# Optimization experiments

Measured on AMD Instinct MI355X. Metric: run time of the kernel, lower is better.

Reference implementation:

```python
import jax, jax.numpy as jnp
import numpy as np

DIM = 256      # dim
DSTATE = 16    # d_state
DCONV = 4      # d_conv
DINNER = 256   # expand=1 -> d_inner = dim (required for B/C Linear shapes to check)
BATCH = 4
NPTS = 4096


def setup_inputs() -> dict:
    key = jax.random.key(0)
    ks = jax.random.split(key, 12)
    s = 0.02
    return {
        "x":      jax.random.normal(ks[0], (BATCH, DIM, NPTS), jnp.float32),
        # in_proj: Conv1d(dim, 2*d_inner, 1)
        "w_in":   jax.random.normal(ks[1], (2 * DINNER, DIM), jnp.float32) * s,
        "b_in":   jnp.zeros((2 * DINNER,), jnp.float32),
        # depthwise conv: Conv1d(d_inner, d_inner, d_conv, groups=d_inner)
        "w_conv": jax.random.normal(ks[2], (DINNER, 1, DCONV), jnp.float32) * s,
        "b_conv": jnp.zeros((DINNER,), jnp.float32),
        # A param; sampled so |A| = exp(A_log) < 1 for a stable 4096-step recurrence
        "A_log":  -jax.random.uniform(ks[3], (DINNER, DSTATE), jnp.float32, 0.1, 3.0),
        "D_skip": jax.random.normal(ks[4], (DINNER,), jnp.float32),
        # B/C Linear(dim, d_state, bias=False) weights [d_state, dim]
        "Bw":     jax.random.normal(ks[5], (DSTATE, DIM), jnp.float32) * s,
        "Cw":     jax.random.normal(ks[6], (DSTATE, DIM), jnp.float32) * s,
        # out_proj: Conv1d(d_inner, dim, 1)
        "w_out":  jax.random.normal(ks[7], (DIM, DINNER), jnp.float32) * s,
        "b_out":  jnp.zeros((DIM,), jnp.float32),
        "gamma":  jnp.ones((DIM,), jnp.float32),
        "beta":   jnp.zeros((DIM,), jnp.float32),
    }


def _forward(x, w_in, b_in, w_conv, b_conv, A_log, D_skip, Bw, Cw, w_out, b_out, gamma, beta):
    B, C, N = x.shape
    residual = jnp.swapaxes(x, 1, 2)                       # [B,N,C]
    # 1x1 conv in_proj on [B,C,N]
    xp = jnp.einsum('bcn,oc->bon', x, w_in) + b_in[:, None]  # [B,2*Di,N]
    x1, z = jnp.split(xp, 2, axis=1)                       # each [B,Di,N]
    # depthwise causal conv (torch pad=d_conv-1 both sides then truncate [:N])
    xc = jax.lax.conv_general_dilated(
        x1, w_conv, window_strides=(1,), padding=[(DCONV - 1, 0)],
        feature_group_count=DINNER,
        dimension_numbers=('NCH', 'OIH', 'NCH')) + b_conv[:, None]
    xs = jax.nn.silu(xc)                                   # [B,Di,N]
    A = -jnp.exp(A_log)                                    # [Di,S]
    xT = jnp.swapaxes(xs, 1, 2)                            # [B,N,Di]
    Bm = xT @ Bw.T                                         # [B,N,S]
    Cm = xT @ Cw.T                                         # [B,N,S]
    delta = jax.nn.sigmoid(jnp.swapaxes(z, 1, 2))          # [B,N,Di]
    dB = delta[..., None] * Bm[:, :, None, :]              # [B,N,Di,S]

    def step(h, t):
        dB_t, C_t, x_t = t                                 # [B,Di,S],[B,S],[B,Di]
        h = A * h + dB_t                                   # diagonal SSM update
        y = jnp.einsum('bds,bs->bd', h, C_t) + D_skip * x_t
        return h, y

    h0 = jnp.zeros((B, DINNER, DSTATE), x.dtype)
    _, ys = jax.lax.scan(
        step, h0,
        (jnp.swapaxes(dB, 0, 1), jnp.swapaxes(Cm, 0, 1), jnp.swapaxes(xT, 0, 1)))
    x_ssm = jnp.transpose(ys, (1, 2, 0))                   # [B,Di,N]
    out = jnp.einsum('bdn,cd->bcn', x_ssm, w_out) + b_out[:, None]  # [B,C,N]
    out = jnp.swapaxes(out, 1, 2) + residual               # [B,N,C]
    mu = out.mean(-1, keepdims=True)
    var = out.var(-1, keepdims=True)
    out = (out - mu) / jnp.sqrt(var + 1e-5) * gamma + beta  # LayerNorm over C
    return jnp.swapaxes(out, 1, 2)                          # [B,C,N]


def reference(x, w_in, b_in, w_conv, b_conv, A_log, D_skip, Bw, Cw, w_out, b_out, gamma, beta):
    return _forward(x, w_in, b_in, w_conv, b_conv, A_log, D_skip, Bw, Cw, w_out, b_out, gamma, beta)
```

## Files before the change

kernel.cpp:

```cpp
#include <hip/hip_runtime.h>
#include <math.h>

#define NPTS 4096
#define LDA  264
#define S_R1  0
#define S_DT  18480
#define S_BML 35376
#define S_CML 37936
#define SMEM_SZ 40496

typedef __bf16 bf16x8 __attribute__((ext_vector_type(8)));
typedef __bf16 bf16x4 __attribute__((ext_vector_type(4)));
typedef float  f32x4  __attribute__((ext_vector_type(4)));
typedef float  f32x2  __attribute__((ext_vector_type(2)));

#define PK_MUL(d, s0, s1)  asm("v_pk_mul_f32 %0, %1, %2" : "=v"(d) : "v"(s0), "v"(s1))
#define PK_FMA(d, s0, s2)  asm("v_pk_fma_f32 %0, %1, %0, %2" : "+v"(d) : "v"(s0), "v"(s2))
#define PK_FMA3(d, s0, s1) asm("v_pk_fma_f32 %0, %1, %2, %0" : "+v"(d) : "v"(s0), "v"(s1))

__device__ __forceinline__ float sigmoidf_(float v) {
  return __fdividef(1.f, 1.f + __expf(-v));
}
__device__ __forceinline__ f32x2 lo2(float4 v) { f32x2 r; r[0] = v.x; r[1] = v.y; return r; }
__device__ __forceinline__ f32x2 hi2(float4 v) { f32x2 r; r[0] = v.z; r[1] = v.w; return r; }

__global__ __launch_bounds__(256) void k_prep(const float* __restrict__ w_in,
                                              const float* __restrict__ w_out,
                                              const float* __restrict__ Bw,
                                              const float* __restrict__ Cw,
                                              __bf16* __restrict__ wbi,
                                              __bf16* __restrict__ wbo,
                                              __bf16* __restrict__ wbB,
                                              __bf16* __restrict__ wbC) {
  int i = blockIdx.x * 256 + threadIdx.x;
  const float* src; __bf16* dst; int off;
  if (i < 32768)      { src = w_in;  dst = wbi; off = i; }
  else if (i < 49152) { src = w_out; dst = wbo; off = i - 32768; }
  else if (i < 50176) { src = Bw;    dst = wbB; off = i - 49152; }
  else                { src = Cw;    dst = wbC; off = i - 50176; }
  float4 v = *(const float4*)&src[off << 2];
  bf16x4 p;
  p[0] = (__bf16)v.x; p[1] = (__bf16)v.y; p[2] = (__bf16)v.z; p[3] = (__bf16)v.w;
  *(bf16x4*)&dst[off << 2] = p;
}

__global__ __launch_bounds__(512, 4) void k_partA(const float* __restrict__ x,
                                                  const __bf16* __restrict__ wbi,
                                                  const float* __restrict__ b_in,
                                                  const float* __restrict__ wconv,
                                                  const float* __restrict__ bconv,
                                                  const float* __restrict__ A_log,
                                                  const __bf16* __restrict__ wbB,
                                                  const __bf16* __restrict__ wbC,
                                                  __bf16* __restrict__ dG,
                                                  __bf16* __restrict__ xsG,
                                                  float* __restrict__ BGg,
                                                  float* __restrict__ CGg,
                                                  float* __restrict__ E) {
  extern __shared__ unsigned char smem[];
  __bf16* R1  = (__bf16*)(smem + S_R1);
  __bf16* bdt = (__bf16*)(smem + S_DT);
  float*  Bml = (float*) (smem + S_BML);
  float*  Cml = (float*) (smem + S_CML);

  const int tid = threadIdx.x, lane = tid & 63, w = tid >> 6;
  const int b = blockIdx.y, cx = blockIdx.x, t0 = cx << 5;
  const int mrow = lane & 15, klane = (lane >> 4) << 3;
  const int r4 = (lane >> 4) << 2;
  const int ds = tid >> 1, sh = (tid & 1) << 3;

  f32x2 a01, a23, a45, a67;
  {
    float4 A0 = *(const float4*)&A_log[(ds << 4) + sh];
    float4 A1 = *(const float4*)&A_log[(ds << 4) + sh + 4];
    a01[0] = -__expf(A0.x); a01[1] = -__expf(A0.y);
    a23[0] = -__expf(A0.z); a23[1] = -__expf(A0.w);
    a45[0] = -__expf(A1.x); a45[1] = -__expf(A1.y);
    a67[0] = -__expf(A1.z); a67[1] = -__expf(A1.w);
  }

  {
    const int c = tid >> 1;
    const size_t xrow = (size_t)(b * 256 + c) * NPTS;
    #pragma unroll
    for (int r = 0; r < 4; ++r) {
      int fg = (tid & 1) + (r << 1);
      int t = t0 + (fg << 2);
      float4 v = *(const float4*)&x[xrow + t];
      int i0 = 3 + (fg << 2);
      R1[(i0 + 0) * LDA + c] = (__bf16)v.x;
      R1[(i0 + 1) * LDA + c] = (__bf16)v.y;
      R1[(i0 + 2) * LDA + c] = (__bf16)v.z;
      R1[(i0 + 3) * LDA + c] = (__bf16)v.w;
    }
    if (tid < 256) {
      int t = t0 - 4;
      float4 v = make_float4(0.f, 0.f, 0.f, 0.f);
      if (t >= 0) v = *(const float4*)&x[(size_t)(b * 256 + tid) * NPTS + t];
      R1[0 * LDA + tid] = (__bf16)v.y;
      R1[1 * LDA + tid] = (__bf16)v.z;
      R1[2 * LDA + tid] = (__bf16)v.w;
    }
  }
  const __bf16* wZ0 = &wbi[(size_t)(256 + (w << 5) + mrow) * 256 + klane];
  const __bf16* wZ1 = wZ0 + 16 * 256;
  bf16x8 z0v = *(const bf16x8*)&wZ0[0];
  bf16x8 z1v = *(const bf16x8*)&wZ1[0];
  __syncthreads();

  {
    f32x4 acc[2][2] = {};
    for (int k0 = 0; k0 < 256; k0 += 32) {
      bf16x8 af0 = z0v, af1 = z1v;
      int kn = (k0 + 32) & 255;
      z0v = *(const bf16x8*)&wZ0[kn];
      z1v = *(const bf16x8*)&wZ1[kn];
      #pragma unroll
      for (int ni = 0; ni < 2; ++ni) {
        bf16x8 bx = *(bf16x8*)&R1[(3 + (ni << 4) + mrow) * LDA + k0 + klane];
        acc[0][ni] = __builtin_amdgcn_mfma_f32_16x16x32_bf16(af0, bx, acc[0][ni], 0, 0, 0);
        acc[1][ni] = __builtin_amdgcn_mfma_f32_16x16x32_bf16(af1, bx, acc[1][ni], 0, 0, 0);
      }
    }
    #pragma unroll
    for (int mi = 0; mi < 2; ++mi) {
      int d = (w << 5) + (mi << 4) + r4;
      float4 bi = *(const float4*)&b_in[256 + d];
      float bia[4] = {bi.x, bi.y, bi.z, bi.w};
      #pragma unroll
      for (int ni = 0; ni < 2; ++ni) {
        int j = (ni << 4) + mrow;
        bf16x4 p;
        #pragma unroll
        for (int rg = 0; rg < 4; ++rg)
          p[rg] = (__bf16)sigmoidf_(acc[mi][ni][rg] + bia[rg]);
        *(bf16x4*)&bdt[j * LDA + d] = p;
      }
    }
  }

  {
    const __bf16* wX0 = &wbi[(size_t)((w << 5) + mrow) * 256 + klane];
    const __bf16* wX1 = wX0 + 16 * 256;
    bf16x8 x0v = *(const bf16x8*)&wX0[0];
    bf16x8 x1v = *(const bf16x8*)&wX1[0];
    f32x4 acc[2][3] = {};
    const int n0s[3] = {0, 16, 19};
    for (int k0 = 0; k0 < 256; k0 += 32) {
      bf16x8 af0 = x0v, af1 = x1v;
      int kn = (k0 + 32) & 255;
      x0v = *(const bf16x8*)&wX0[kn];
      x1v = *(const bf16x8*)&wX1[kn];
      #pragma unroll
      for (int ni = 0; ni < 3; ++ni) {
        bf16x8 bx = *(bf16x8*)&R1[(n0s[ni] + mrow) * LDA + k0 + klane];
        acc[0][ni] = __builtin_amdgcn_mfma_f32_16x16x32_bf16(af0, bx, acc[0][ni], 0, 0, 0);
        acc[1][ni] = __builtin_amdgcn_mfma_f32_16x16x32_bf16(af1, bx, acc[1][ni], 0, 0, 0);
      }
    }
    __syncthreads();
    #pragma unroll
    for (int mi = 0; mi < 2; ++mi) {
      int d = (w << 5) + (mi << 4) + r4;
      float4 bi = *(const float4*)&b_in[d];
      float bia[4] = {bi.x, bi.y, bi.z, bi.w};
      #pragma unroll
      for (int ni = 0; ni < 3; ++ni) {
        int i = n0s[ni] + mrow;
        bool ok = (t0 - 3 + i) >= 0;
        bf16x4 p;
        #pragma unroll
        for (int rg = 0; rg < 4; ++rg) {
          float v = acc[mi][ni][rg] + bia[rg];
          p[rg] = ok ? (__bf16)v : (__bf16)0.f;
        }
        *(bf16x4*)&R1[i * LDA + d] = p;
      }
    }
  }
  #pragma unroll
  for (int r = 0; r < 2; ++r) {
    int idx = (r << 9) + tid;
    int row = idx >> 5, colg = (idx & 31) << 3;
    *(uint4*)&dG[((size_t)(b * NPTS + t0 + row)) * 256 + colg] =
        *(uint4*)&bdt[row * LDA + colg];
  }
  __syncthreads();

  const int mat = w >> 1, n0bc = (w & 1) << 4;
  const __bf16* WrBC = (mat ? wbC : wbB) + mrow * 256 + klane;
  bf16x8 wv = {};
  if (w < 4) wv = *(const bf16x8*)&WrBC[0];

  {
    const int d = tid & 255, seg = tid >> 8;
    const int j0 = seg << 4;
    const float4 wc = *(const float4*)&wconv[d << 2];
    const float bcv = bconv[d];
    float m3 = (float)R1[(j0 + 0) * LDA + d];
    float m2 = (float)R1[(j0 + 1) * LDA + d];
    float m1 = (float)R1[(j0 + 2) * LDA + d];
    float xc_n = (float)R1[(j0 + 3) * LDA + d];
    float d0 = 0.f, d1 = 0.f, d2 = 0.f;
    #pragma unroll
    for (int i2 = 0; i2 < 16; ++i2) {
      float xc = xc_n;
      xc_n = (float)R1[(j0 + (i2 == 15 ? 18 : i2 + 4)) * LDA + d];
      float cv = fmaf(wc.x, m3, fmaf(wc.y, m2, fmaf(wc.z, m1, fmaf(wc.w, xc, bcv))));
      float sv = cv * sigmoidf_(cv);
      if (seg && i2 == 0)      d0 = sv;
      else if (seg && i2 == 1) d1 = sv;
      else if (seg && i2 == 2) d2 = sv;
      else R1[(j0 + i2) * LDA + d] = (__bf16)sv;
      m3 = m2; m2 = m1; m1 = xc;
    }
    __syncthreads();
    if (seg) {
      R1[(j0 + 0) * LDA + d] = (__bf16)d0;
      R1[(j0 + 1) * LDA + d] = (__bf16)d1;
      R1[(j0 + 2) * LDA + d] = (__bf16)d2;
    }
  }
  __syncthreads();

  if (w < 4) {
    f32x4 accb = {};
    for (int k0 = 0; k0 < 256; k0 += 32) {
      bf16x8 av = wv;
      int kn = (k0 + 32) & 255;
      wv = *(const bf16x8*)&WrBC[kn];
      bf16x8 bv = *(bf16x8*)&R1[(n0bc + mrow) * LDA + k0 + klane];
      accb = __builtin_amdgcn_mfma_f32_16x16x32_bf16(av, bv, accb, 0, 0, 0);
    }
    float* dst = mat ? Cml : Bml;
    int j = n0bc + mrow;
    #pragma unroll
    for (int rg = 0; rg < 4; ++rg)
      dst[j * 20 + r4 + rg] = accb[rg];
  } else {
    const int tid2 = tid - 256;
    #pragma unroll
    for (int r = 0; r < 4; ++r) {
      int idx = (r << 8) + tid2;
      int row = idx >> 5, colg = (idx & 31) << 3;
      *(uint4*)&xsG[((size_t)(b * NPTS + t0 + row)) * 256 + colg] =
          *(uint4*)&R1[row * LDA + colg];
    }
  }
  __syncthreads();

  {
    int j = tid >> 4, s = tid & 15;
    size_t gi = ((size_t)(b * 128 + cx) << 9) + tid;
    BGg[gi] = Bml[j * 20 + s];
    CGg[gi] = Cml[j * 20 + s];
  }

  f32x2 h01 = {0.f, 0.f}, h23 = {0.f, 0.f}, h45 = {0.f, 0.f}, h67 = {0.f, 0.f};
  {
    float u_n = (float)bdt[0 * LDA + ds];
    float4 b0_n = *(float4*)&Bml[0 * 20 + sh];
    float4 b1_n = *(float4*)&Bml[0 * 20 + sh + 4];
    #pragma unroll
    for (int j = 0; j < 32; ++j) {
      float u = u_n; float4 b0 = b0_n, b1 = b1_n;
      int jn = (j + 1) & 31;
      u_n = (float)bdt[jn * LDA + ds];
      b0_n = *(float4*)&Bml[jn * 20 + sh];
      b1_n = *(float4*)&Bml[jn * 20 + sh + 4];
      f32x2 u2; u2[0] = u; u2[1] = u;
      f32x2 t;
      PK_MUL(t, u2, lo2(b0)); PK_FMA(h01, a01, t);
      PK_MUL(t, u2, hi2(b0)); PK_FMA(h23, a23, t);
      PK_MUL(t, u2, lo2(b1)); PK_FMA(h45, a45, t);
      PK_MUL(t, u2, hi2(b1)); PK_FMA(h67, a67, t);
    }
  }
  {
    float* Ep = E + ((size_t)(b * 128 + cx) << 12) + (ds << 4) + sh;
    float4 e0, e1;
    e0.x = h01[0]; e0.y = h01[1]; e0.z = h23[0]; e0.w = h23[1];
    e1.x = h45[0]; e1.y = h45[1]; e1.z = h67[0]; e1.w = h67[1];
    *(float4*)&Ep[0] = e0;
    *(float4*)&Ep[4] = e1;
  }
}

__global__ __launch_bounds__(512, 4) void k_partB(const float* __restrict__ x,
                                                  const float* __restrict__ A_log,
                                                  const float* __restrict__ Dsk,
                                                  const __bf16* __restrict__ wbo,
                                                  const float* __restrict__ b_out,
                                                  const float* __restrict__ gamma,
                                                  const float* __restrict__ beta,
                                                  const __bf16* __restrict__ dG,
                                                  const __bf16* __restrict__ xsG,
                                                  const float* __restrict__ BGg,
                                                  const float* __restrict__ CGg,
                                                  const float* __restrict__ E,
                                                  float* __restrict__ out) {
  extern __shared__ unsigned char smem[];
  __bf16* R1  = (__bf16*)(smem + S_R1);
  __bf16* bdt = (__bf16*)(smem + S_DT);
  float*  Bml = (float*) (smem + S_BML);
  float*  Cml = (float*) (smem + S_CML);
  float*  Ct  = (float*) (smem + S_R1);

  const int tid = threadIdx.x, lane = tid & 63, w = tid >> 6;
  const int b = blockIdx.y, cx = blockIdx.x, t0 = cx << 5;
  const int mrow = lane & 15, klane = (lane >> 4) << 3;
  const int r4 = (lane >> 4) << 2;
  const int ds = tid >> 1, sh = (tid & 1) << 3;

  const __bf16* wO0 = &wbo[(size_t)((w << 5) + mrow) * 256 + klane];
  const __bf16* wO1 = wO0 + 16 * 256;
  bf16x8 o0v = *(const bf16x8*)&wO0[0];
  bf16x8 o1v = *(const bf16x8*)&wO1[0];

  #pragma unroll
  for (int r = 0; r < 2; ++r) {
    int idx = (r << 9) + tid;
    int row = idx >> 5, colg = (idx & 31) << 3;
    size_t gsrc = ((size_t)(b * NPTS + t0 + row)) * 256 + colg;
    *(uint4*)&bdt[row * LDA + colg] = *(const uint4*)&dG[gsrc];
    *(uint4*)&R1[row * LDA + colg]  = *(const uint4*)&xsG[gsrc];
  }
  {
    int j = tid >> 4, s = tid & 15;
    size_t gi = ((size_t)(b * 128 + cx) << 9) + tid;
    Bml[j * 20 + s] = BGg[gi];
    Cml[j * 20 + s] = CGg[gi];
  }

  f32x2 a01, a23, a45, a67, a32_01, a32_23, a32_45, a32_67;
  {
    float4 A0 = *(const float4*)&A_log[(ds << 4) + sh];
    float4 A1 = *(const float4*)&A_log[(ds << 4) + sh + 4];
    a01[0] = -__expf(A0.x); a01[1] = -__expf(A0.y);
    a23[0] = -__expf(A0.z); a23[1] = -__expf(A0.w);
    a45[0] = -__expf(A1.x); a45[1] = -__expf(A1.y);
    a67[0] = -__expf(A1.z); a67[1] = -__expf(A1.w);
    a32_01[0] = __expf(32.f * A0.x); a32_01[1] = __expf(32.f * A0.y);
    a32_23[0] = __expf(32.f * A0.z); a32_23[1] = __expf(32.f * A0.w);
    a32_45[0] = __expf(32.f * A1.x); a32_45[1] = __expf(32.f * A1.y);
    a32_67[0] = __expf(32.f * A1.z); a32_67[1] = __expf(32.f * A1.w);
  }
  const float Dv = Dsk[ds];

  f32x2 h01, h23, h45, h67;
  {
    const float* Eb = E + ((size_t)(b * 128) << 12) + (ds << 4) + sh;
    float4 z4 = make_float4(0.f, 0.f, 0.f, 0.f);
    float4 e1a = z4, e1b = z4, e2a = z4, e2b = z4, e3a = z4, e3b = z4;
    if (cx >= 1) { e1a = *(const float4*)&Eb[(size_t)(cx - 1) << 12];
                   e1b = *(const float4*)&Eb[((size_t)(cx - 1) << 12) + 4]; }
    if (cx >= 2) { e2a = *(const float4*)&Eb[(size_t)(cx - 2) << 12];
                   e2b = *(const float4*)&Eb[((size_t)(cx - 2) << 12) + 4]; }
    if (cx >= 3) { e3a = *(const float4*)&Eb[(size_t)(cx - 3) << 12];
                   e3b = *(const float4*)&Eb[((size_t)(cx - 3) << 12) + 4]; }
    f32x2 t01 = lo2(e2a); PK_FMA3(t01, a32_01, lo2(e3a));
    f32x2 t23 = hi2(e2a); PK_FMA3(t23, a32_23, hi2(e3a));
    f32x2 t45 = lo2(e2b); PK_FMA3(t45, a32_45, lo2(e3b));
    f32x2 t67 = hi2(e2b); PK_FMA3(t67, a32_67, hi2(e3b));
    h01 = lo2(e1a); PK_FMA3(h01, a32_01, t01);
    h23 = hi2(e1a); PK_FMA3(h23, a32_23, t23);
    h45 = lo2(e1b); PK_FMA3(h45, a32_45, t45);
    h67 = hi2(e1b); PK_FMA3(h67, a32_67, t67);
  }
  __syncthreads();

  {
    float u_n = (float)bdt[0 * LDA + ds];
    float4 b0_n = *(float4*)&Bml[0 * 20 + sh];
    float4 b1_n = *(float4*)&Bml[0 * 20 + sh + 4];
    float4 c0_n = *(float4*)&Cml[0 * 20 + sh];
    float4 c1_n = *(float4*)&Cml[0 * 20 + sh + 4];
    #pragma unroll
    for (int j = 0; j < 32; ++j) {
      float u = u_n; float4 b0 = b0_n, b1 = b1_n, c0 = c0_n, c1 = c1_n;
      int jn = (j + 1) & 31;
      u_n = (float)bdt[jn * LDA + ds];
      b0_n = *(float4*)&Bml[jn * 20 + sh];
      b1_n = *(float4*)&Bml[jn * 20 + sh + 4];
      c0_n = *(float4*)&Cml[jn * 20 + sh];
      c1_n = *(float4*)&Cml[jn * 20 + sh + 4];
      f32x2 u2; u2[0] = u; u2[1] = u;
      f32x2 t, pa, pb;
      PK_MUL(t, u2, lo2(b0)); PK_FMA(h01, a01, t);
      PK_MUL(t, u2, hi2(b0)); PK_FMA(h23, a23, t);
      PK_MUL(t, u2, lo2(b1)); PK_FMA(h45, a45, t);
      PK_MUL(t, u2, hi2(b1)); PK_FMA(h67, a67, t);
      PK_MUL(pa, h01, lo2(c0)); PK_FMA3(pa, h23, hi2(c0));
      PK_MUL(pb, h45, lo2(c1)); PK_FMA3(pb, h67, hi2(c1));
      float yv = pa[0] + pa[1] + pb[0] + pb[1];
      yv += __shfl_xor(yv, 1);
      if ((tid & 1) == 0) {
        float xv = (float)R1[j * LDA + ds];
        R1[j * LDA + ds] = (__bf16)fmaf(Dv, xv, yv);
      }
    }
  }
  __syncthreads();

  float4 xv[4]; float bo4[4];
  {
    f32x4 acc[2][2] = {};
    for (int k0 = 0; k0 < 256; k0 += 32) {
      bf16x8 af0 = o0v, af1 = o1v;
      int kn = (k0 + 32) & 255;
      o0v = *(const bf16x8*)&wO0[kn];
      o1v = *(const bf16x8*)&wO1[kn];
      bf16x8 bx0 = *(bf16x8*)&R1[(0 + mrow) * LDA + k0 + klane];
      bf16x8 bx1 = *(bf16x8*)&R1[(16 + mrow) * LDA + k0 + klane];
      acc[0][0] = __builtin_amdgcn_mfma_f32_16x16x32_bf16(af0, bx0, acc[0][0], 0, 0, 0);
      acc[0][1] = __builtin_amdgcn_mfma_f32_16x16x32_bf16(af0, bx1, acc[0][1], 0, 0, 0);
      acc[1][0] = __builtin_amdgcn_mfma_f32_16x16x32_bf16(af1, bx0, acc[1][0], 0, 0, 0);
      acc[1][1] = __builtin_amdgcn_mfma_f32_16x16x32_bf16(af1, bx1, acc[1][1], 0, 0, 0);
    }
    #pragma unroll
    for (int r = 0; r < 4; ++r) {
      int idx = (r << 9) + tid;
      int c = idx >> 3, t4 = (idx & 7) << 2;
      xv[r] = *(const float4*)&x[((size_t)(b * 256 + c)) * NPTS + t0 + t4];
      bo4[r] = b_out[c];
    }
    __syncthreads();
    const int o0w = w << 5;
    #pragma unroll
    for (int mi = 0; mi < 2; ++mi)
      #pragma unroll
      for (int ni = 0; ni < 2; ++ni) {
        int t = (ni << 4) + mrow;
        int o = o0w + (mi << 4) + r4;
        #pragma unroll
        for (int rg = 0; rg < 4; ++rg)
          Ct[t * 257 + o + rg] = acc[mi][ni][rg];
      }
  }
  __syncthreads();

  #pragma unroll
  for (int r = 0; r < 4; ++r) {
    int idx = (r << 9) + tid;
    int c = idx >> 3, t4 = (idx & 7) << 2;
    Ct[(t4 + 0) * 257 + c] += xv[r].x + bo4[r];
    Ct[(t4 + 1) * 257 + c] += xv[r].y + bo4[r];
    Ct[(t4 + 2) * 257 + c] += xv[r].z + bo4[r];
    Ct[(t4 + 3) * 257 + c] += xv[r].w + bo4[r];
  }
  float g[4], be[4];
  #pragma unroll
  for (int j = 0; j < 4; ++j) {
    g[j]  = gamma[lane + 64 * j];
    be[j] = beta[lane + 64 * j];
  }
  __syncthreads();
  #pragma unroll
  for (int rr = 0; rr < 4; ++rr) {
    int t = (w << 2) + rr;
    float v[4];
    float sum = 0.f, sq2 = 0.f;
    #pragma unroll
    for (int j = 0; j < 4; ++j) {
      v[j] = Ct[t * 257 + lane + 64 * j];
      sum += v[j];
      sq2 += v[j] * v[j];
    }
    #pragma unroll
    for (int m = 1; m < 64; m <<= 1) {
      sum += __shfl_xor(sum, m);
      sq2 += __shfl_xor(sq2, m);
    }
    float mean = sum * (1.f / 256.f);
    float var = sq2 * (1.f / 256.f) - mean * mean;
    float rstd = rsqrtf(var + 1e-5f);
    #pragma unroll
    for (int j = 0; j < 4; ++j)
      Ct[t * 257 + lane + 64 * j] = (v[j] - mean) * rstd * g[j] + be[j];
  }
  __syncthreads();
  #pragma unroll
  for (int p = 0; p < 4; ++p) {
    int c = (p << 6) + (tid >> 3), t4 = (tid & 7) << 2;
    float4 o;
    o.x = Ct[(t4 + 0) * 257 + c];
    o.y = Ct[(t4 + 1) * 257 + c];
    o.z = Ct[(t4 + 2) * 257 + c];
    o.w = Ct[(t4 + 3) * 257 + c];
    *(float4*)&out[((size_t)(b * 256 + c)) * NPTS + t0 + t4] = o;
  }
}

extern "C" void kernel_launch(void* const* d_in, const int* in_sizes, int n_in,
                              void* d_out, int out_size, void* d_ws, size_t ws_size,
                              hipStream_t stream) {
  const float* x     = (const float*)d_in[0];
  const float* w_in  = (const float*)d_in[1];
  const float* b_in  = (const float*)d_in[2];
  const float* wconv = (const float*)d_in[3];
  const float* bconv = (const float*)d_in[4];
  const float* A_log = (const float*)d_in[5];
  const float* Dsk   = (const float*)d_in[6];
  const float* Bw    = (const float*)d_in[7];
  const float* Cw    = (const float*)d_in[8];
  const float* w_out = (const float*)d_in[9];
  const float* b_out = (const float*)d_in[10];
  const float* gamma = (const float*)d_in[11];
  const float* beta  = (const float*)d_in[12];
  float* ws = (float*)d_ws;
  __bf16* wbi  = (__bf16*)(ws + 0);
  __bf16* wbo  = (__bf16*)(ws + 65536);
  __bf16* wbB  = (__bf16*)(ws + 98304);
  __bf16* wbC  = (__bf16*)(ws + 100352);
  float*  Ebuf = ws + 102400;
  __bf16* dG   = (__bf16*)(ws + 2199552);
  __bf16* xsG  = (__bf16*)(ws + 4296704);
  float*  BGg  = ws + 6393856;
  float*  CGg  = ws + 6656000;
  float* out = (float*)d_out;

  k_prep<<<200, 256, 0, stream>>>(w_in, w_out, Bw, Cw, wbi, wbo, wbB, wbC);
  k_partA<<<dim3(128, 4), 512, SMEM_SZ, stream>>>(x, wbi, b_in, wconv, bconv, A_log,
                                                  wbB, wbC, dG, xsG, BGg, CGg, Ebuf);
  k_partB<<<dim3(128, 4), 512, SMEM_SZ, stream>>>(x, A_log, Dsk, wbo, b_out, gamma, beta,
                                                  dG, xsG, BGg, CGg, Ebuf, out);
}
```

Before: 141.3 us.

## Fuse partA and partB into one kernel with inter-block flag synchronization

Merges the two chunked-scan kernels into a single kernel. Each block keeps its delta, xs and B/C tiles in shared memory instead of writing them to global memory and reloading them. Blocks publish their chunk-end state via a per-chunk flag and spin-wait on the previous three chunks before the carry-in combine. The A^32 factor is now computed by repeated squaring. This removes large global round-trips and one launch, but relies on all 512 blocks being co-resident or scheduled in order to avoid deadlock, and it adds a memset.

```diff
diff --git a/kernel.cpp b/kernel.cpp
--- a/kernel.cpp
+++ b/kernel.cpp
@@ -44,24 +44,28 @@
   *(bf16x4*)&dst[off << 2] = p;
 }
 
-__global__ __launch_bounds__(512, 4) void k_partA(const float* __restrict__ x,
-                                                  const __bf16* __restrict__ wbi,
-                                                  const float* __restrict__ b_in,
-                                                  const float* __restrict__ wconv,
-                                                  const float* __restrict__ bconv,
-                                                  const float* __restrict__ A_log,
-                                                  const __bf16* __restrict__ wbB,
-                                                  const __bf16* __restrict__ wbC,
-                                                  __bf16* __restrict__ dG,
-                                                  __bf16* __restrict__ xsG,
-                                                  float* __restrict__ BGg,
-                                                  float* __restrict__ CGg,
-                                                  float* __restrict__ E) {
+__global__ __launch_bounds__(512, 4) void k_mega(const float* __restrict__ x,
+                                                 const __bf16* __restrict__ wbi,
+                                                 const float* __restrict__ b_in,
+                                                 const float* __restrict__ wconv,
+                                                 const float* __restrict__ bconv,
+                                                 const float* __restrict__ A_log,
+                                                 const float* __restrict__ Dsk,
+                                                 const __bf16* __restrict__ wbB,
+                                                 const __bf16* __restrict__ wbC,
+                                                 const __bf16* __restrict__ wbo,
+                                                 const float* __restrict__ b_out,
+                                                 const float* __restrict__ gamma,
+                                                 const float* __restrict__ beta,
+                                                 float* __restrict__ E,
+                                                 int* __restrict__ flag,
+                                                 float* __restrict__ out) {
   extern __shared__ unsigned char smem[];
   __bf16* R1  = (__bf16*)(smem + S_R1);
   __bf16* bdt = (__bf16*)(smem + S_DT);
   float*  Bml = (float*) (smem + S_BML);
   float*  Cml = (float*) (smem + S_CML);
+  float*  Ct  = (float*) (smem + S_R1);
 
   const int tid = threadIdx.x, lane = tid & 63, w = tid >> 6;
   const int b = blockIdx.y, cx = blockIdx.x, t0 = cx << 5;
@@ -78,6 +82,7 @@
     a45[0] = -__expf(A1.x); a45[1] = -__expf(A1.y);
     a67[0] = -__expf(A1.z); a67[1] = -__expf(A1.w);
   }
+  const float Dv = Dsk[ds];
 
   {
     const int c = tid >> 1;
@@ -178,13 +183,6 @@
       }
     }
   }
-  #pragma unroll
-  for (int r = 0; r < 2; ++r) {
-    int idx = (r << 9) + tid;
-    int row = idx >> 5, colg = (idx & 31) << 3;
-    *(uint4*)&dG[((size_t)(b * NPTS + t0 + row)) * 256 + colg] =
-        *(uint4*)&bdt[row * LDA + colg];
-  }
   __syncthreads();
 
   const int mat = w >> 1, n0bc = (w & 1) << 4;
@@ -237,24 +235,12 @@
     #pragma unroll
     for (int rg = 0; rg < 4; ++rg)
       dst[j * 20 + r4 + rg] = accb[rg];
-  } else {
-    const int tid2 = tid - 256;
-    #pragma unroll
-    for (int r = 0; r < 4; ++r) {
-      int idx = (r << 8) + tid2;
-      int row = idx >> 5, colg = (idx & 31) << 3;
-      *(uint4*)&xsG[((size_t)(b * NPTS + t0 + row)) * 256 + colg] =
-          *(uint4*)&R1[row * LDA + colg];
-    }
-  }
-  __syncthreads();
-
-  {
-    int j = tid >> 4, s = tid & 15;
-    size_t gi = ((size_t)(b * 128 + cx) << 9) + tid;
-    BGg[gi] = Bml[j * 20 + s];
-    CGg[gi] = Cml[j * 20 + s];
-  }
+  }
+  const __bf16* wO0 = &wbo[(size_t)((w << 5) + mrow) * 256 + klane];
+  const __bf16* wO1 = wO0 + 16 * 256;
+  bf16x8 o0v = *(const bf16x8*)&wO0[0];
+  bf16x8 o1v = *(const bf16x8*)&wO1[0];
+  __syncthreads();
 
   f32x2 h01 = {0.f, 0.f}, h23 = {0.f, 0.f}, h45 = {0.f, 0.f}, h67 = {0.f, 0.f};
   {
@@ -284,71 +270,42 @@
     *(float4*)&Ep[0] = e0;
     *(float4*)&Ep[4] = e1;
   }
-}
-
-__global__ __launch_bounds__(512, 4) void k_partB(const float* __restrict__ x,
-                                                  const float* __restrict__ A_log,
-                                                  const float* __restrict__ Dsk,
-                                                  const __bf16* __restrict__ wbo,
-                                                  const float* __restrict__ b_out,
-                                                  const float* __restrict__ gamma,
-                                                  const float* __restrict__ beta,
-                                                  const __bf16* __restrict__ dG,
-                                                  const __bf16* __restrict__ xsG,
-                                                  const float* __restrict__ BGg,
-                                                  const float* __restrict__ CGg,
-                                                  const float* __restrict__ E,
-                                                  float* __restrict__ out) {
-  extern __shared__ unsigned char smem[];
-  __bf16* R1  = (__bf16*)(smem + S_R1);
-  __bf16* bdt = (__bf16*)(smem + S_DT);
-  float*  Bml = (float*) (smem + S_BML);
-  float*  Cml = (float*) (smem + S_CML);
-  float*  Ct  = (float*) (smem + S_R1);
-
-  const int tid = threadIdx.x, lane = tid & 63, w = tid >> 6;
-  const int b = blockIdx.y, cx = blockIdx.x, t0 = cx << 5;
-  const int mrow = lane & 15, klane = (lane >> 4) << 3;
-  const int r4 = (lane >> 4) << 2;
-  const int ds = tid >> 1, sh = (tid & 1) << 3;
-
-  const __bf16* wO0 = &wbo[(size_t)((w << 5) + mrow) * 256 + klane];
-  const __bf16* wO1 = wO0 + 16 * 256;
-  bf16x8 o0v = *(const bf16x8*)&wO0[0];
-  bf16x8 o1v = *(const bf16x8*)&wO1[0];
-
+  __syncthreads();
+  if (tid == 0) {
+    __threadfence();
+    atomicExch(&flag[b * 128 + cx], 1);
+  }
+
+  float4 xv[4]; float bo4[4];
   #pragma unroll
-  for (int r = 0; r < 2; ++r) {
+  for (int r = 0; r < 4; ++r) {
     int idx = (r << 9) + tid;
-    int row = idx >> 5, colg = (idx & 31) << 3;
-    size_t gsrc = ((size_t)(b * NPTS + t0 + row)) * 256 + colg;
-    *(uint4*)&bdt[row * LDA + colg] = *(const uint4*)&dG[gsrc];
-    *(uint4*)&R1[row * LDA + colg]  = *(const uint4*)&xsG[gsrc];
-  }
-  {
-    int j = tid >> 4, s = tid & 15;
-    size_t gi = ((size_t)(b * 128 + cx) << 9) + tid;
-    Bml[j * 20 + s] = BGg[gi];
-    Cml[j * 20 + s] = CGg[gi];
-  }
-
-  f32x2 a01, a23, a45, a67, a32_01, a32_23, a32_45, a32_67;
-  {
-    float4 A0 = *(const float4*)&A_log[(ds << 4) + sh];
-    float4 A1 = *(const float4*)&A_log[(ds << 4) + sh + 4];
-    a01[0] = -__expf(A0.x); a01[1] = -__expf(A0.y);
-    a23[0] = -__expf(A0.z); a23[1] = -__expf(A0.w);
-    a45[0] = -__expf(A1.x); a45[1] = -__expf(A1.y);
-    a67[0] = -__expf(A1.z); a67[1] = -__expf(A1.w);
-    a32_01[0] = __expf(32.f * A0.x); a32_01[1] = __expf(32.f * A0.y);
-    a32_23[0] = __expf(32.f * A0.z); a32_23[1] = __expf(32.f * A0.w);
-    a32_45[0] = __expf(32.f * A1.x); a32_45[1] = __expf(32.f * A1.y);
-    a32_67[0] = __expf(32.f * A1.z); a32_67[1] = __expf(32.f * A1.w);
-  }
-  const float Dv = Dsk[ds];
-
-  f32x2 h01, h23, h45, h67;
-  {
+    int c = idx >> 3, t4 = (idx & 7) << 2;
+    xv[r] = *(const float4*)&x[((size_t)(b * 256 + c)) * NPTS + t0 + t4];
+    bo4[r] = b_out[c];
+  }
+
+  if (tid < 3) {
+    int src = cx - 1 - tid;
+    if (src >= 0) {
+      while (__hip_atomic_load(&flag[b * 128 + src], __ATOMIC_RELAXED,
+                               __HIP_MEMORY_SCOPE_AGENT) == 0) {
+        __builtin_amdgcn_s_sleep(1);
+      }
+    }
+  }
+  __syncthreads();
+  __threadfence();
+
+  {
+    f32x2 a32_01 = a01, a32_23 = a23, a32_45 = a45, a32_67 = a67;
+    #pragma unroll
+    for (int q = 0; q < 5; ++q) {
+      PK_MUL(a32_01, a32_01, a32_01);
+      PK_MUL(a32_23, a32_23, a32_23);
+      PK_MUL(a32_45, a32_45, a32_45);
+      PK_MUL(a32_67, a32_67, a32_67);
+    }
     const float* Eb = E + ((size_t)(b * 128) << 12) + (ds << 4) + sh;
     float4 z4 = make_float4(0.f, 0.f, 0.f, 0.f);
     float4 e1a = z4, e1b = z4, e2a = z4, e2b = z4, e3a = z4, e3b = z4;
@@ -367,7 +324,6 @@
     h45 = lo2(e1b); PK_FMA3(h45, a32_45, t45);
     h67 = hi2(e1b); PK_FMA3(h67, a32_67, t67);
   }
-  __syncthreads();
 
   {
     float u_n = (float)bdt[0 * LDA + ds];
@@ -395,14 +351,13 @@
       float yv = pa[0] + pa[1] + pb[0] + pb[1];
       yv += __shfl_xor(yv, 1);
       if ((tid & 1) == 0) {
-        float xv = (float)R1[j * LDA + ds];
-        R1[j * LDA + ds] = (__bf16)fmaf(Dv, xv, yv);
-      }
-    }
-  }
-  __syncthreads();
-
-  float4 xv[4]; float bo4[4];
+        float xvs = (float)R1[j * LDA + ds];
+        R1[j * LDA + ds] = (__bf16)fmaf(Dv, xvs, yv);
+      }
+    }
+  }
+  __syncthreads();
+
   {
     f32x4 acc[2][2] = {};
     for (int k0 = 0; k0 < 256; k0 += 32) {
@@ -416,13 +371,6 @@
       acc[0][1] = __builtin_amdgcn_mfma_f32_16x16x32_bf16(af0, bx1, acc[0][1], 0, 0, 0);
       acc[1][0] = __builtin_amdgcn_mfma_f32_16x16x32_bf16(af1, bx0, acc[1][0], 0, 0, 0);
       acc[1][1] = __builtin_amdgcn_mfma_f32_16x16x32_bf16(af1, bx1, acc[1][1], 0, 0, 0);
-    }
-    #pragma unroll
-    for (int r = 0; r < 4; ++r) {
-      int idx = (r << 9) + tid;
-      int c = idx >> 3, t4 = (idx & 7) << 2;
-      xv[r] = *(const float4*)&x[((size_t)(b * 256 + c)) * NPTS + t0 + t4];
-      bo4[r] = b_out[c];
     }
     __syncthreads();
     const int o0w = w << 5;
@@ -513,15 +461,12 @@
   __bf16* wbB  = (__bf16*)(ws + 98304);
   __bf16* wbC  = (__bf16*)(ws + 100352);
   float*  Ebuf = ws + 102400;
-  __bf16* dG   = (__bf16*)(ws + 2199552);
-  __bf16* xsG  = (__bf16*)(ws + 4296704);
-  float*  BGg  = ws + 6393856;
-  float*  CGg  = ws + 6656000;
+  int*    flag = (int*)(ws + 2199552);
   float* out = (float*)d_out;
 
+  hipMemsetAsync(flag, 0, 4 * 128 * sizeof(int), stream);
   k_prep<<<200, 256, 0, stream>>>(w_in, w_out, Bw, Cw, wbi, wbo, wbB, wbC);
-  k_partA<<<dim3(128, 4), 512, SMEM_SZ, stream>>>(x, wbi, b_in, wconv, bconv, A_log,
-                                                  wbB, wbC, dG, xsG, BGg, CGg, Ebuf);
-  k_partB<<<dim3(128, 4), 512, SMEM_SZ, stream>>>(x, A_log, Dsk, wbo, b_out, gamma, beta,
-                                                  dG, xsG, BGg, CGg, Ebuf, out);
+  k_mega<<<dim3(128, 4), 512, SMEM_SZ, stream>>>(x, wbi, b_in, wconv, bconv, A_log,
+                                                 Dsk, wbB, wbC, wbo, b_out, gamma, beta,
+                                                 Ebuf, flag, out);
 }
```

New measurement: 250.2 us. 77.0% more time.
